# Performance work log

Hardware: AMD Instinct MI355X
Metric: run time of the kernel (lower is better)

Reference implementation:

```python
import jax, jax.numpy as jnp
import numpy as np

D_MODEL = 1024
N_HEAD = 16
D_HEAD = 64
M_FEAT = 128  # d_kernel_map


def _gen_projection_matrix(m, d, rng):
    # Performer-style: stacked orthogonal blocks scaled by chi-distributed row norms
    blocks = []
    for _ in range(m // d):
        q, _ = np.linalg.qr(rng.standard_normal((d, d)))
        blocks.append(q.T)
    rem = m % d
    if rem > 0:
        q, _ = np.linalg.qr(rng.standard_normal((d, d)))
        blocks.append(q.T[:rem])
    mat = np.vstack(blocks)
    multiplier = np.linalg.norm(rng.standard_normal((m, d)), axis=1, keepdims=True)
    return (mat * multiplier).astype(np.float32)


def setup_inputs() -> dict:
    key = jax.random.key(0)
    ks = jax.random.split(key, 6)
    B, L = 4, 4096
    rng = np.random.default_rng(0)
    hd = N_HEAD * D_HEAD
    x = jax.random.normal(ks[0], (B, L, D_MODEL), dtype=jnp.float32)
    pos_ft = jax.random.normal(ks[1], (B, L, D_MODEL), dtype=jnp.float32)
    pos_ft_slopes = jax.random.normal(ks[2], (B, L, D_MODEL), dtype=jnp.float32)
    W_v = jax.random.normal(ks[3], (D_MODEL, hd), dtype=jnp.float32) / np.sqrt(D_MODEL)
    W_o = jax.random.normal(ks[4], (hd, D_MODEL), dtype=jnp.float32) / np.sqrt(hd)
    pos_ft_weight = jax.random.normal(ks[5], (D_MODEL, hd), dtype=jnp.float32)
    pos_ft_scale = jnp.ones((1, 1, N_HEAD, 1), dtype=jnp.float32)
    head_range = 1.0 / N_HEAD
    offs = (np.arange(0, 1.0, head_range) + head_range / 2.0).astype(np.float32)
    pos_ft_offsets = jnp.asarray(offs).reshape(1, 1, N_HEAD, 1)
    proj = jnp.asarray(_gen_projection_matrix(M_FEAT, D_HEAD, rng))
    return {"x": x, "pos_ft": pos_ft, "pos_ft_slopes": pos_ft_slopes,
            "W_v": W_v, "W_o": W_o, "pos_ft_weight": pos_ft_weight,
            "pos_ft_scale": pos_ft_scale, "pos_ft_offsets": pos_ft_offsets,
            "proj": proj}


def _fourier_kernel(data, proj):
    # data: [B,L,H,D]; proj: [M,D] -> features [B,L,H,2M]
    data_normalizer = 1.0 / data.shape[-1] ** 0.25
    ratio = 1.0 / proj.shape[0] ** 0.5
    data_dash = jnp.einsum('blhd,md->blhm', data_normalizer * data, proj)
    return jnp.concatenate([ratio * jnp.sin(data_dash), ratio * jnp.cos(data_dash)], axis=-1)


def reference(x, pos_ft, pos_ft_slopes, W_v, W_o, pos_ft_weight, pos_ft_scale, pos_ft_offsets, proj):
    B, L, _ = x.shape
    v = (x @ W_v).reshape(B, L, N_HEAD, D_HEAD)
    pos_proj = (pos_ft @ pos_ft_weight).reshape(B, L, N_HEAD, D_HEAD)
    slope_proj = (pos_ft_slopes @ pos_ft_weight).reshape(B, L, N_HEAD, D_HEAD)
    query_pos = pos_ft_scale * pos_proj
    key_pos = query_pos + pos_ft_offsets * (pos_ft_scale * slope_proj)
    q_prime = _fourier_kernel(query_pos, proj)   # [B,L,H,2M]
    k_prime = _fourier_kernel(key_pos, proj)
    kv = jnp.einsum('blhm,blhd->bhmd', k_prime, v)
    z = jnp.einsum('blhm,bhmd->blhd', q_prime, kv)
    norm_factor = jnp.linalg.norm(slope_proj, axis=-1, keepdims=True) / float(L)
    z = (z * norm_factor).reshape(B, L, N_HEAD * D_HEAD)
    # dropout is identity in eval mode
    return z @ W_o
```

## Files before the change

kernel.cpp:

```cpp
#include <hip/hip_runtime.h>
#include <hip/hip_bf16.h>
#include <stdint.h>


typedef _Float16 hx8 __attribute__((ext_vector_type(8)));
typedef _Float16 hx4 __attribute__((ext_vector_type(4)));
typedef float    fx4 __attribute__((ext_vector_type(4)));

#define H_   16
#define D_   64
#define L_   4096
#define B_   4
#define KV_SPLIT 16

__device__ __forceinline__ void g2l16(const _Float16* g, _Float16* l) {
  __builtin_amdgcn_global_load_lds(
      (const __attribute__((address_space(1))) void*)g,
      (__attribute__((address_space(3))) void*)l, 16, 0, 0);
}

__global__ __launch_bounds__(256) void wt_k(const float* __restrict__ W,
                                            _Float16* __restrict__ WT) {
  __shared__ float tile[64][65];
  int t = threadIdx.x; int c = t & 63; int r0 = t >> 6;
  int bx = blockIdx.x * 64, by = blockIdx.y * 64;
  for (int r = r0; r < 64; r += 4) tile[r][c] = W[(long)(by + r) * 1024 + bx + c];
  __syncthreads();
  for (int r = r0; r < 64; r += 4)
    WT[(long)(bx + r) * 1024 + by + c] = (_Float16)tile[c][r];
}

__global__ __launch_bounds__(256) void wpf3_k(const float* __restrict__ W,
                                              _Float16* __restrict__ WT3) {
  __shared__ float tile[64][65];
  int t = threadIdx.x; int c = t & 63; int r0 = t >> 6;
  int bx = blockIdx.x * 64, by = blockIdx.y * 64;
  for (int r = r0; r < 64; r += 4) tile[r][c] = W[(long)(by + r) * 1024 + bx + c];
  __syncthreads();
  for (int r = r0; r < 64; r += 4) {
    float x = tile[c][r];
    _Float16 hi = (_Float16)x;
    _Float16 lo = (_Float16)(x - (float)hi);
    long base = (long)(bx + r) * 3072 + by + c;
    WT3[base] = hi; WT3[base + 1024] = hi; WT3[base + 2048] = lo;
  }
}

__global__ __launch_bounds__(256) void proj3_k(const float* __restrict__ proj,
                                               _Float16* __restrict__ proj3T) {
  int i = blockIdx.x * 256 + threadIdx.x;
  if (i >= 8192) return;
  int m = i >> 6, d = i & 63;
  float p = 0.35355339059327373f * proj[i];
  _Float16 hi = (_Float16)p;
  _Float16 lo = (_Float16)(p - (float)hi);
  proj3T[(long)m * 192 + d]       = hi;
  proj3T[(long)m * 192 + 64 + d]  = hi;
  proj3T[(long)m * 192 + 128 + d] = lo;
}

__global__ __launch_bounds__(256) void zero_k(float* __restrict__ p, int n4) {
  int i = blockIdx.x * 256 + threadIdx.x;
  int stride = gridDim.x * 256;
  fx4 z = {0.f, 0.f, 0.f, 0.f};
  for (; i < n4; i += stride) ((fx4*)p)[i] = z;
}

__global__ __launch_bounds__(256) void cast_out_f16_k(const float* __restrict__ in,
                                                      _Float16* __restrict__ out, int n) {
  int i = blockIdx.x * 256 + threadIdx.x;
  int stride = gridDim.x * 256;
  for (; i < n; i += stride) out[i] = (_Float16)in[i];
}

__global__ __launch_bounds__(256) void cvt_hilo_k(const float* __restrict__ in,
                                                  _Float16* __restrict__ out) {
  long i = (long)blockIdx.x * 256 + threadIdx.x;
  long idx = i * 8;
  int row = (int)(idx >> 10), c = (int)(idx & 1023);
  fx4 a = *(const fx4*)&in[idx];
  fx4 b = *(const fx4*)&in[idx + 4];
  hx8 hi, lo;
#pragma unroll
  for (int e = 0; e < 4; ++e) {
    _Float16 h0 = (_Float16)a[e]; hi[e] = h0;     lo[e]     = (_Float16)(a[e] - (float)h0);
    _Float16 h1 = (_Float16)b[e]; hi[4 + e] = h1; lo[4 + e] = (_Float16)(b[e] - (float)h1);
  }
  *(hx8*)&out[(long)row * 2048 + c]        = hi;
  *(hx8*)&out[(long)row * 2048 + 1024 + c] = lo;
}

__global__ __launch_bounds__(256) void cvt16_k(const float* __restrict__ in,
                                               _Float16* __restrict__ out, long n8) {
  long i = (long)blockIdx.x * 256 + threadIdx.x;
  if (i >= n8) return;
  long idx = i * 8;
  fx4 a = *(const fx4*)&in[idx];
  fx4 b = *(const fx4*)&in[idx + 4];
  hx8 h;
#pragma unroll
  for (int e = 0; e < 4; ++e) { h[e] = (_Float16)a[e]; h[4 + e] = (_Float16)b[e]; }
  *(hx8*)&out[idx] = h;
}

template<int BM, int BN, int AMODE, int SECSH, int EPI, typename OUT_T>
__global__ __launch_bounds__(256) void gemm_bt_k(
    const void* __restrict__ Av, const _Float16* __restrict__ BT,
    OUT_T* __restrict__ C, int K, int lda, int ldb, int ldc,
    long sAb, long sAh, long sBb, long sBh, long sCb, long sCh,
    const float* __restrict__ norms, const float* __restrict__ scp,
    const float* __restrict__ ofp, const float* __restrict__ Pprev,
    float* __restrict__ nout)
{
  __shared__ __align__(16) _Float16 sA[BM * 64];
  __shared__ __align__(16) _Float16 sB[BN * 64];
  const int t = threadIdx.x;
  const int lane = t & 63;
  const int w = t >> 6;
  const int wm = w >> 1, wn = w & 1;
  const int by = blockIdx.x, bx = blockIdx.y, bz = blockIdx.z;
  long aoff = (long)(bz >> 4) * sAb + (long)(bz & 15) * sAh;
  BT += (long)(bz >> 4) * sBb + (long)(bz & 15) * sBh;
  C  += (long)(bz >> 4) * sCb + (long)(bz & 15) * sCh;
  const _Float16* A16 = (const _Float16*)Av + aoff;
  const float*    A32 = (const float*)Av + aoff;
  if constexpr (EPI == 4) {
    if (bz & 15) {
      if constexpr (AMODE == 4) A16 = (const _Float16*)Pprev + aoff;
      else                      A32 = Pprev + aoff;
    }
  }
  constexpr int WTM = BM / 32, WTN = BN / 32;
  fx4 acc[WTM][WTN];
#pragma unroll
  for (int i = 0; i < WTM; ++i)
#pragma unroll
    for (int j = 0; j < WTN; ++j) acc[i][j] = (fx4){0.f, 0.f, 0.f, 0.f};

  for (int k0 = 0; k0 < K; k0 += 64) {
    __syncthreads();
    if constexpr (AMODE == 0 || AMODE == 4) {
      int cb;
      if constexpr (AMODE == 4) {
        int sec = k0 >> SECSH;
        cb = (k0 & ((1 << SECSH) - 1)) + (sec == 1 ? (1 << SECSH) : 0);
      } else cb = k0;
#pragma unroll
      for (int i = 0; i < BM / 32; ++i) {
        int s = i * 256 + t; int row = s >> 3; int kc = (s & 7) ^ (row & 7);
        g2l16(&A16[(long)(by * BM + row) * lda + cb + kc * 8],
              &sA[(long)(i * 256 + (w << 6)) * 8]);
      }
    } else {
      int mode, cs;
      if constexpr (AMODE >= 2) { mode = k0 >> SECSH; cs = k0 & ((1 << SECSH) - 1); }
      else                      { mode = 0;           cs = k0;                      }
#pragma unroll
      for (int i = 0; i < BM / 32; ++i) {
        int s = i * 256 + t; int row = s >> 3; int kc = (s & 7) ^ (row & 7);
        const float* src = A32 + (long)(by * BM + row) * lda + cs + kc * 8;
        fx4 v0 = *(const fx4*)src;
        fx4 v1 = *(const fx4*)(src + 4);
        if constexpr (AMODE == 3) {
          if (bz & 15) {
            const float* src2 = src + sAb;
            fx4 w0 = *(const fx4*)src2;
            fx4 w1 = *(const fx4*)(src2 + 4);
#pragma unroll
            for (int e = 0; e < 4; ++e) { v0[e] += w0[e]; v1[e] += w1[e]; }
          }
        }
        hx8 hv;
        if (mode != 1) {
#pragma unroll
          for (int e = 0; e < 4; ++e) { hv[e] = (_Float16)v0[e]; hv[4 + e] = (_Float16)v1[e]; }
        } else {
#pragma unroll
          for (int e = 0; e < 4; ++e) {
            _Float16 h0 = (_Float16)v0[e]; hv[e]     = (_Float16)(v0[e] - (float)h0);
            _Float16 h1 = (_Float16)v1[e]; hv[4 + e] = (_Float16)(v1[e] - (float)h1);
          }
        }
        *(hx8*)&sA[s * 8] = hv;
      }
    }
#pragma unroll
    for (int i = 0; i < BN / 32; ++i) {
      int s = i * 256 + t; int row = s >> 3; int kc = (s & 7) ^ (row & 7);
      g2l16(&BT[(long)(bx * BN + row) * ldb + k0 + kc * 8],
            &sB[(long)(i * 256 + (w << 6)) * 8]);
    }
    __syncthreads();
#pragma unroll
    for (int kk = 0; kk < 64; kk += 32) {
      hx8 af[WTM], bf[WTN];
      int kcb = (kk >> 3) + (lane >> 4);
#pragma unroll
      for (int i = 0; i < WTM; ++i) {
        int r = wm * (BM / 2) + i * 16 + (lane & 15);
        af[i] = *(const hx8*)&sA[(r * 8 + (kcb ^ (r & 7))) * 8];
      }
#pragma unroll
      for (int j = 0; j < WTN; ++j) {
        int r = wn * (BN / 2) + j * 16 + (lane & 15);
        bf[j] = *(const hx8*)&sB[(r * 8 + (kcb ^ (r & 7))) * 8];
      }
#pragma unroll
      for (int i = 0; i < WTM; ++i)
#pragma unroll
        for (int j = 0; j < WTN; ++j)
          acc[i][j] = __builtin_amdgcn_mfma_f32_16x16x32_f16(af[i], bf[j], acc[i][j], 0, 0, 0);
    }
  }
  if constexpr (EPI == 0) {
#pragma unroll
    for (int i = 0; i < WTM; ++i) {
#pragma unroll
      for (int j = 0; j < WTN; ++j) {
        int rowb = by * BM + wm * (BM / 2) + i * 16 + ((lane >> 4) << 2);
        int col  = bx * BN + wn * (BN / 2) + j * 16 + (lane & 15);
#pragma unroll
        for (int r = 0; r < 4; ++r)
          C[(long)(rowb + r) * ldc + col] = (OUT_T)acc[i][j][r];
      }
    }
  } else if constexpr (EPI == 1) {
    const float inv2pi = 0.15915494309189535f;
    const float ratio  = 0.08838834764831845f;
    const bool useN = ((bz & 15) == 0);
#pragma unroll
    for (int i = 0; i < WTM; ++i) {
#pragma unroll
      for (int j = 0; j < WTN; ++j) {
        int rowb = by * BM + wm * (BM / 2) + i * 16 + ((lane >> 4) << 2);
        int col  = bx * BN + wn * (BN / 2) + j * 16 + (lane & 15);
#pragma unroll
        for (int r = 0; r < 4; ++r) {
          int row = rowb + r;
          float rn = ratio * (useN ? norms[row] : 1.0f);
          long ob = ((long)(row & 15) * 4096 + (row >> 4)) * 256;
          float v = acc[i][j][r] * inv2pi;
          v -= floorf(v);
          C[ob + col]       = (OUT_T)(rn * __builtin_amdgcn_sinf(v));
          C[ob + 128 + col] = (OUT_T)(rn * __builtin_amdgcn_cosf(v));
        }
      }
    }
  } else if constexpr (EPI == 2) {
    const int h = ((bx * BN) >> 6) + wn;
    const float sc = scp[h];
#pragma unroll
    for (int i = 0; i < WTM; ++i) {
#pragma unroll
      for (int j = 0; j < WTN; ++j) {
        int rowb = by * BM + wm * (BM / 2) + i * 16 + ((lane >> 4) << 2);
        int col  = bx * BN + wn * (BN / 2) + j * 16 + (lane & 15);
#pragma unroll
        for (int r = 0; r < 4; ++r)
          C[(long)(rowb + r) * ldc + col] = (OUT_T)(sc * acc[i][j][r]);
      }
    }
  } else {
    const int h = ((bx * BN) >> 6) + wn;
    const float sc = scp[h];
    if ((bz & 15) == 0) {
#pragma unroll
      for (int i = 0; i < WTM; ++i) {
#pragma unroll
        for (int j = 0; j < WTN; ++j) {
          int rowb = by * BM + wm * (BM / 2) + i * 16 + ((lane >> 4) << 2);
          int col  = bx * BN + wn * (BN / 2) + j * 16 + (lane & 15);
#pragma unroll
          for (int r = 0; r < 4; ++r)
            C[(long)(rowb + r) * ldc + col] = (OUT_T)(sc * acc[i][j][r]);
        }
      }
    } else {
      const float osc = ofp[h] * sc;
#pragma unroll
      for (int i = 0; i < WTM; ++i) {
        float sq[4] = {0.f, 0.f, 0.f, 0.f};
        int rowb = by * BM + wm * (BM / 2) + i * 16 + ((lane >> 4) << 2);
#pragma unroll
        for (int j = 0; j < WTN; ++j) {
          int col = bx * BN + wn * (BN / 2) + j * 16 + (lane & 15);
#pragma unroll
          for (int r = 0; r < 4; ++r) {
            float a = acc[i][j][r];
            sq[r] += a * a;
            C[(long)(rowb + r) * ldc + col] = (OUT_T)(osc * a);
          }
        }
#pragma unroll
        for (int r = 0; r < 4; ++r) {
          float s = sq[r];
          s += __shfl_xor(s, 1); s += __shfl_xor(s, 2);
          s += __shfl_xor(s, 4); s += __shfl_xor(s, 8);
          if ((lane & 15) == 0)
            nout[(long)(rowb + r) * 16 + h] = sqrtf(s) * (1.0f / 4096.0f);
        }
      }
    }
  }
}

__global__ __launch_bounds__(256) void kv_k(const _Float16* __restrict__ Kp,
                                            const _Float16* __restrict__ Vhb,
                                            float* __restrict__ kvacc)
{
  __shared__ __align__(16) _Float16 sK[256 * 72];
  __shared__ __align__(16) _Float16 sV[64 * 72];
  const int t = threadIdx.x, lane = t & 63, w = t >> 6;
  const int h = blockIdx.x;
  const int l0 = blockIdx.y * (L_ / KV_SPLIT);
  fx4 acc[4][4];
#pragma unroll
  for (int i = 0; i < 4; ++i)
#pragma unroll
    for (int j = 0; j < 4; ++j) acc[i][j] = (fx4){0.f, 0.f, 0.f, 0.f};
  const _Float16* Kbase = Kp + (long)h * L_ * 256;
  for (int kt = 0; kt < L_ / KV_SPLIT; kt += 64) {
    __syncthreads();
#pragma unroll
    for (int i = 0; i < 8; ++i) {
      int mc = w + 4 * i;
      hx8 vv = *(const hx8*)&Kbase[(long)(l0 + kt + lane) * 256 + mc * 8];
#pragma unroll
      for (int e = 0; e < 8; ++e) sK[(mc * 8 + e) * 72 + lane] = vv[e];
    }
#pragma unroll
    for (int i = 0; i < 2; ++i) {
      int dc = w + 4 * i;
      hx8 vv = *(const hx8*)&Vhb[(long)(l0 + kt + lane) * 1024 + h * 64 + dc * 8];
#pragma unroll
      for (int e = 0; e < 8; ++e) sV[(dc * 8 + e) * 72 + lane] = vv[e];
    }
    __syncthreads();
#pragma unroll
    for (int kk = 0; kk < 64; kk += 32) {
      hx8 af[4], bf[4];
      int lfr = kk + ((lane >> 4) << 3);
#pragma unroll
      for (int i = 0; i < 4; ++i)
        af[i] = *(const hx8*)&sV[(i * 16 + (lane & 15)) * 72 + lfr];
#pragma unroll
      for (int j = 0; j < 4; ++j)
        bf[j] = *(const hx8*)&sK[(w * 64 + j * 16 + (lane & 15)) * 72 + lfr];
#pragma unroll
      for (int i = 0; i < 4; ++i)
#pragma unroll
        for (int j = 0; j < 4; ++j)
          acc[i][j] = __builtin_amdgcn_mfma_f32_16x16x32_f16(af[i], bf[j], acc[i][j], 0, 0, 0);
    }
  }
  float* obase = kvacc + (long)h * (64 * 256);
#pragma unroll
  for (int i = 0; i < 4; ++i)
#pragma unroll
    for (int j = 0; j < 4; ++j) {
      int d0 = i * 16 + ((lane >> 4) << 2);
      int m  = w * 64 + j * 16 + (lane & 15);
#pragma unroll
      for (int r = 0; r < 4; ++r)
        atomicAdd(&obase[(long)(d0 + r) * 256 + m], acc[i][j][r]);
    }
}

extern "C" void kernel_launch(void* const* d_in, const int* in_sizes, int n_in,
                              void* d_out, int out_size, void* d_ws, size_t ws_size,
                              hipStream_t stream) {
  const float* x     = (const float*)d_in[0];
  const float* pos   = (const float*)d_in[1];
  const float* slp   = (const float*)d_in[2];
  const float* Wv    = (const float*)d_in[3];
  const float* Wo    = (const float*)d_in[4];
  const float* Wpf   = (const float*)d_in[5];
  const float* scale = (const float*)d_in[6];
  const float* offs  = (const float*)d_in[7];
  const float* proj  = (const float*)d_in[8];
  float* out = (float*)d_out;
  char* ws = (char*)d_ws;

  size_t o = 0;
  auto alloc = [&](size_t bytes) { char* p = ws + o; o += (bytes + 255) & ~(size_t)255; return p; };
  float*    Pb     = (float*)alloc(33554432);
  float*    Sb     = (float*)alloc(33554432);
  _Float16* qpr    = (_Float16*)alloc(33554432);
  _Float16* kpr    = (_Float16*)alloc(33554432);
  _Float16* Vh     = (_Float16*)alloc(33554432);
  _Float16* Zb     = (_Float16*)alloc(33554432);
  _Float16* WvT    = (_Float16*)alloc(2097152);
  _Float16* WoT    = (_Float16*)alloc(2097152);
  _Float16* Wpf3T  = (_Float16*)alloc(6291456);
  _Float16* proj3T = (_Float16*)alloc(49152);
  float*    normsB = (float*)alloc(524288);
  float*    kvacc  = (float*)alloc(4194304);
  _Float16* kvh    = (_Float16*)alloc(2097152);
  _Float16* ph2 = qpr;
  _Float16* sh2 = kpr;
  _Float16* xh  = Zb;
  (void)ws_size; (void)in_sizes; (void)n_in; (void)out_size;

  wt_k<<<dim3(16, 16), 256, 0, stream>>>(Wv, WvT);
  wt_k<<<dim3(16, 16), 256, 0, stream>>>(Wo, WoT);
  wpf3_k<<<dim3(16, 16), 256, 0, stream>>>(Wpf, Wpf3T);
  proj3_k<<<32, 256, 0, stream>>>(proj, proj3T);
  zero_k<<<256, 256, 0, stream>>>(kvacc, 262144);
  cvt16_k<<<8192, 256, 0, stream>>>(x, xh, 2097152);

  gemm_bt_k<128, 128, 0, 0, 0, _Float16><<<dim3(128, 8, 1), 256, 0, stream>>>(
      xh, WvT, Vh, 1024, 1024, 1024, 1024, 0, 0, 0, 0, 0, 0,
      nullptr, nullptr, nullptr, nullptr, nullptr);

  for (int sb = 0; sb < 2; ++sb) {
    const float* pos_sb = pos + (long)sb * 8192 * 1024;
    const float* slp_sb = slp + (long)sb * 8192 * 1024;
    cvt_hilo_k<<<4096, 256, 0, stream>>>(pos_sb, ph2);
    cvt_hilo_k<<<4096, 256, 0, stream>>>(slp_sb, sh2);
    gemm_bt_k<128, 128, 4, 10, 4, float><<<dim3(64, 8, 2), 256, 0, stream>>>(
        ph2, Wpf3T, Pb, 3072, 2048, 3072, 1024, 0, 0, 0, 0, 0, 8388608L,
        nullptr, scale, offs, (const float*)sh2, normsB);

    for (int bb = 0; bb < 2; ++bb) {
      int b = sb * 2 + bb;
      _Float16* Vh_b  = Vh + (long)b * L_ * 1024;
      _Float16* Zb_b  = Zb + (long)b * L_ * 1024;
      float* kvacc_b  = kvacc + (long)b * H_ * 64 * 256;
      _Float16* kvh_b = kvh   + (long)b * H_ * 64 * 256;
      gemm_bt_k<128, 128, 3, 6, 1, _Float16><<<dim3(512, 1, 2), 256, 0, stream>>>(
          Pb + (long)bb * 4194304, proj3T, qpr, 192, 64, 192, 0,
          8388608L, 0L, 0, 0, 0, 16777216L,
          normsB + (long)bb * 65536, nullptr, nullptr, nullptr, nullptr);
      kv_k<<<dim3(16, KV_SPLIT), 256, 0, stream>>>(kpr, Vh_b, kvacc_b);
      cast_out_f16_k<<<1024, 256, 0, stream>>>(kvacc_b, kvh_b, 262144);
      gemm_bt_k<128, 64, 0, 0, 0, _Float16><<<dim3(32, 1, 16), 256, 0, stream>>>(
          qpr, kvh_b, Zb_b, 256, 256, 256, 1024,
          0L, (long)L_ * 256, 0L, 16384L, 0L, 64L,
          nullptr, nullptr, nullptr, nullptr, nullptr);
    }
  }
  gemm_bt_k<128, 128, 0, 0, 0, float><<<dim3(128, 8, 1), 256, 0, stream>>>(
      Zb, WoT, out, 1024, 1024, 1024, 1024, 0, 0, 0, 0, 0, 0,
      nullptr, nullptr, nullptr, nullptr, nullptr);
}
```

Measured before the change: 943.3 us.

## Store position projections as fp16 hi/lo pairs and swizzle kv_k shared-memory layout

The position-projection GEMM now writes its output as fp16 hi/lo pairs in a per-head [row,head,128] layout instead of fp32. The feature GEMM gains a new A mode that loads these fp16 pairs directly through global-to-LDS copies, with a doubled proj6T matrix; for the query half it skips the key-only sections by halving K. This removes the fp32 reads and register conversion from the feature GEMM. The kv_k staging is rewritten so each thread loads four rows and writes 4-wide packed values into an XOR-swizzled shared layout, aiming to cut bank conflicts. The cost is more index arithmetic and a more intricate addressing scheme that has to stay consistent between the producer and consumer kernels.

```diff
diff --git a/kernel.cpp b/kernel.cpp
--- a/kernel.cpp
+++ b/kernel.cpp
@@ -46,17 +46,17 @@
   }
 }
 
-__global__ __launch_bounds__(256) void proj3_k(const float* __restrict__ proj,
-                                               _Float16* __restrict__ proj3T) {
+__global__ __launch_bounds__(256) void proj6_k(const float* __restrict__ proj,
+                                               _Float16* __restrict__ proj6T) {
   int i = blockIdx.x * 256 + threadIdx.x;
   if (i >= 8192) return;
   int m = i >> 6, d = i & 63;
   float p = 0.35355339059327373f * proj[i];
   _Float16 hi = (_Float16)p;
   _Float16 lo = (_Float16)(p - (float)hi);
-  proj3T[(long)m * 192 + d]       = hi;
-  proj3T[(long)m * 192 + 64 + d]  = hi;
-  proj3T[(long)m * 192 + 128 + d] = lo;
+  long b = (long)m * 384 + d;
+  proj6T[b]       = hi; proj6T[b + 64]  = hi; proj6T[b + 128] = lo;
+  proj6T[b + 192] = hi; proj6T[b + 256] = hi; proj6T[b + 320] = lo;
 }
 
 __global__ __launch_bounds__(256) void zero_k(float* __restrict__ p, int n4) {
@@ -120,15 +120,13 @@
   const int wm = w >> 1, wn = w & 1;
   const int by = blockIdx.x, bx = blockIdx.y, bz = blockIdx.z;
   long aoff = (long)(bz >> 4) * sAb + (long)(bz & 15) * sAh;
+  if constexpr (AMODE == 5) aoff = 0;
   BT += (long)(bz >> 4) * sBb + (long)(bz & 15) * sBh;
   C  += (long)(bz >> 4) * sCb + (long)(bz & 15) * sCh;
   const _Float16* A16 = (const _Float16*)Av + aoff;
   const float*    A32 = (const float*)Av + aoff;
   if constexpr (EPI == 4) {
-    if (bz & 15) {
-      if constexpr (AMODE == 4) A16 = (const _Float16*)Pprev + aoff;
-      else                      A32 = Pprev + aoff;
-    }
+    if (bz & 15) A16 = (const _Float16*)Pprev + aoff;
   }
   constexpr int WTM = BM / 32, WTN = BN / 32;
   fx4 acc[WTM][WTN];
@@ -137,13 +135,19 @@
 #pragma unroll
     for (int j = 0; j < WTN; ++j) acc[i][j] = (fx4){0.f, 0.f, 0.f, 0.f};
 
-  for (int k0 = 0; k0 < K; k0 += 64) {
+  int Klim = K;
+  if constexpr (AMODE == 5) { if ((bz & 1) == 0) Klim >>= 1; }
+
+  for (int k0 = 0; k0 < Klim; k0 += 64) {
     __syncthreads();
-    if constexpr (AMODE == 0 || AMODE == 4) {
-      int cb;
+    if constexpr (AMODE == 0 || AMODE == 4 || AMODE == 5) {
+      long cb;
       if constexpr (AMODE == 4) {
         int sec = k0 >> SECSH;
         cb = (k0 & ((1 << SECSH) - 1)) + (sec == 1 ? (1 << SECSH) : 0);
+      } else if constexpr (AMODE == 5) {
+        int sec = k0 >> SECSH;
+        cb = ((sec == 1 || sec == 4) ? 64 : 0) + ((sec >= 3) ? sAb : 0);
       } else cb = k0;
 #pragma unroll
       for (int i = 0; i < BM / 32; ++i) {
@@ -263,16 +267,22 @@
   } else {
     const int h = ((bx * BN) >> 6) + wn;
     const float sc = scp[h];
+    _Float16* C16 = (_Float16*)C;
     if ((bz & 15) == 0) {
 #pragma unroll
       for (int i = 0; i < WTM; ++i) {
 #pragma unroll
         for (int j = 0; j < WTN; ++j) {
           int rowb = by * BM + wm * (BM / 2) + i * 16 + ((lane >> 4) << 2);
-          int col  = bx * BN + wn * (BN / 2) + j * 16 + (lane & 15);
-#pragma unroll
-          for (int r = 0; r < 4; ++r)
-            C[(long)(rowb + r) * ldc + col] = (OUT_T)(sc * acc[i][j][r]);
+          int d    = wn * 0 + j * 16 + (lane & 15);
+#pragma unroll
+          for (int r = 0; r < 4; ++r) {
+            float v = sc * acc[i][j][r];
+            long a = ((long)(rowb + r) * 16 + h) * 128 + d;
+            _Float16 hi = (_Float16)v;
+            C16[a]      = hi;
+            C16[a + 64] = (_Float16)(v - (float)hi);
+          }
         }
       }
     } else {
@@ -283,12 +293,16 @@
         int rowb = by * BM + wm * (BM / 2) + i * 16 + ((lane >> 4) << 2);
 #pragma unroll
         for (int j = 0; j < WTN; ++j) {
-          int col = bx * BN + wn * (BN / 2) + j * 16 + (lane & 15);
+          int d = j * 16 + (lane & 15);
 #pragma unroll
           for (int r = 0; r < 4; ++r) {
-            float a = acc[i][j][r];
-            sq[r] += a * a;
-            C[(long)(rowb + r) * ldc + col] = (OUT_T)(osc * a);
+            float a0 = acc[i][j][r];
+            sq[r] += a0 * a0;
+            float v = osc * a0;
+            long a = ((long)(rowb + r) * 16 + h) * 128 + d;
+            _Float16 hi = (_Float16)v;
+            C16[a]      = hi;
+            C16[a + 64] = (_Float16)(v - (float)hi);
           }
         }
 #pragma unroll
@@ -322,18 +336,36 @@
   for (int kt = 0; kt < L_ / KV_SPLIT; kt += 64) {
     __syncthreads();
 #pragma unroll
-    for (int i = 0; i < 8; ++i) {
-      int mc = w + 4 * i;
-      hx8 vv = *(const hx8*)&Kbase[(long)(l0 + kt + lane) * 256 + mc * 8];
-#pragma unroll
-      for (int e = 0; e < 8; ++e) sK[(mc * 8 + e) * 72 + lane] = vv[e];
-    }
-#pragma unroll
-    for (int i = 0; i < 2; ++i) {
-      int dc = w + 4 * i;
-      hx8 vv = *(const hx8*)&Vhb[(long)(l0 + kt + lane) * 1024 + h * 64 + dc * 8];
-#pragma unroll
-      for (int e = 0; e < 8; ++e) sV[(dc * 8 + e) * 72 + lane] = vv[e];
+    for (int it = 0; it < 2; ++it) {
+      int idx = t + it * 256;
+      int m8 = idx & 31, bl = (idx >> 5) << 2;
+      const _Float16* src = &Kbase[(long)(l0 + kt + bl) * 256 + m8 * 8];
+      hx8 r0 = *(const hx8*)(src);
+      hx8 r1 = *(const hx8*)(src + 256);
+      hx8 r2 = *(const hx8*)(src + 512);
+      hx8 r3 = *(const hx8*)(src + 768);
+      int kx = (m8 & 7) << 4;
+#pragma unroll
+      for (int e = 0; e < 8; ++e) {
+        hx4 v; v[0] = r0[e]; v[1] = r1[e]; v[2] = r2[e]; v[3] = r3[e];
+        int byte = (((m8 * 8 + e) * 72 + bl) * 2) ^ kx;
+        *(hx4*)((char*)sK + byte) = v;
+      }
+    }
+    if (t < 128) {
+      int d8 = t & 7, bl = (t >> 3) << 2;
+      const _Float16* src = &Vhb[(long)(l0 + kt + bl) * 1024 + h * 64 + d8 * 8];
+      hx8 r0 = *(const hx8*)(src);
+      hx8 r1 = *(const hx8*)(src + 1024);
+      hx8 r2 = *(const hx8*)(src + 2048);
+      hx8 r3 = *(const hx8*)(src + 3072);
+      int kx = d8 << 4;
+#pragma unroll
+      for (int e = 0; e < 8; ++e) {
+        hx4 v; v[0] = r0[e]; v[1] = r1[e]; v[2] = r2[e]; v[3] = r3[e];
+        int byte = (((d8 * 8 + e) * 72 + bl) * 2) ^ kx;
+        *(hx4*)((char*)sV + byte) = v;
+      }
     }
     __syncthreads();
 #pragma unroll
@@ -341,11 +373,17 @@
       hx8 af[4], bf[4];
       int lfr = kk + ((lane >> 4) << 3);
 #pragma unroll
-      for (int i = 0; i < 4; ++i)
-        af[i] = *(const hx8*)&sV[(i * 16 + (lane & 15)) * 72 + lfr];
-#pragma unroll
-      for (int j = 0; j < 4; ++j)
-        bf[j] = *(const hx8*)&sK[(w * 64 + j * 16 + (lane & 15)) * 72 + lfr];
+      for (int i = 0; i < 4; ++i) {
+        int r = i * 16 + (lane & 15);
+        af[i] = *(const hx8*)((const char*)sV +
+                ((((r * 72 + lfr) * 2)) ^ (((r >> 3) & 7) << 4)));
+      }
+#pragma unroll
+      for (int j = 0; j < 4; ++j) {
+        int r = w * 64 + j * 16 + (lane & 15);
+        bf[j] = *(const hx8*)((const char*)sK +
+                ((((r * 72 + lfr) * 2)) ^ (((r >> 3) & 7) << 4)));
+      }
 #pragma unroll
       for (int i = 0; i < 4; ++i)
 #pragma unroll
@@ -383,8 +421,8 @@
 
   size_t o = 0;
   auto alloc = [&](size_t bytes) { char* p = ws + o; o += (bytes + 255) & ~(size_t)255; return p; };
-  float*    Pb     = (float*)alloc(33554432);
-  float*    Sb     = (float*)alloc(33554432);
+  _Float16* Pb2    = (_Float16*)alloc(33554432);
+  _Float16* Sb2    = (_Float16*)alloc(33554432);
   _Float16* qpr    = (_Float16*)alloc(33554432);
   _Float16* kpr    = (_Float16*)alloc(33554432);
   _Float16* Vh     = (_Float16*)alloc(33554432);
@@ -392,19 +430,19 @@
   _Float16* WvT    = (_Float16*)alloc(2097152);
   _Float16* WoT    = (_Float16*)alloc(2097152);
   _Float16* Wpf3T  = (_Float16*)alloc(6291456);
-  _Float16* proj3T = (_Float16*)alloc(49152);
+  _Float16* proj6T = (_Float16*)alloc(98304);
   float*    normsB = (float*)alloc(524288);
   float*    kvacc  = (float*)alloc(4194304);
   _Float16* kvh    = (_Float16*)alloc(2097152);
   _Float16* ph2 = qpr;
   _Float16* sh2 = kpr;
   _Float16* xh  = Zb;
-  (void)ws_size; (void)in_sizes; (void)n_in; (void)out_size;
+  (void)Sb2; (void)ws_size; (void)in_sizes; (void)n_in; (void)out_size;
 
   wt_k<<<dim3(16, 16), 256, 0, stream>>>(Wv, WvT);
   wt_k<<<dim3(16, 16), 256, 0, stream>>>(Wo, WoT);
   wpf3_k<<<dim3(16, 16), 256, 0, stream>>>(Wpf, Wpf3T);
-  proj3_k<<<32, 256, 0, stream>>>(proj, proj3T);
+  proj6_k<<<32, 256, 0, stream>>>(proj, proj6T);
   zero_k<<<256, 256, 0, stream>>>(kvacc, 262144);
   cvt16_k<<<8192, 256, 0, stream>>>(x, xh, 2097152);
 
@@ -417,8 +455,8 @@
     const float* slp_sb = slp + (long)sb * 8192 * 1024;
     cvt_hilo_k<<<4096, 256, 0, stream>>>(pos_sb, ph2);
     cvt_hilo_k<<<4096, 256, 0, stream>>>(slp_sb, sh2);
-    gemm_bt_k<128, 128, 4, 10, 4, float><<<dim3(64, 8, 2), 256, 0, stream>>>(
-        ph2, Wpf3T, Pb, 3072, 2048, 3072, 1024, 0, 0, 0, 0, 0, 8388608L,
+    gemm_bt_k<128, 128, 4, 10, 4, _Float16><<<dim3(64, 8, 2), 256, 0, stream>>>(
+        ph2, Wpf3T, Pb2, 3072, 2048, 3072, 128, 0, 0, 0, 0, 0, 16777216L,
         nullptr, scale, offs, (const float*)sh2, normsB);
 
     for (int bb = 0; bb < 2; ++bb) {
@@ -427,9 +465,9 @@
       _Float16* Zb_b  = Zb + (long)b * L_ * 1024;
       float* kvacc_b  = kvacc + (long)b * H_ * 64 * 256;
       _Float16* kvh_b = kvh   + (long)b * H_ * 64 * 256;
-      gemm_bt_k<128, 128, 3, 6, 1, _Float16><<<dim3(512, 1, 2), 256, 0, stream>>>(
-          Pb + (long)bb * 4194304, proj3T, qpr, 192, 64, 192, 0,
-          8388608L, 0L, 0, 0, 0, 16777216L,
+      gemm_bt_k<128, 128, 5, 6, 1, _Float16><<<dim3(512, 1, 2), 256, 0, stream>>>(
+          Pb2 + (long)bb * 8388608, proj6T, qpr, 384, 128, 384, 0,
+          16777216L , 0L, 0, 0, 0, 16777216L,
           normsB + (long)bb * 65536, nullptr, nullptr, nullptr, nullptr);
       kv_k<<<dim3(16, KV_SPLIT), 256, 0, stream>>>(kpr, Vh_b, kvacc_b);
       cast_out_f16_k<<<1024, 256, 0, stream>>>(kvacc_b, kvh_b, 262144);
```

New measurement: 896.7 us. 4.9% less time.
